# Kernel optimization log

Hardware: AMD Instinct MI355X
Metric: run time of the kernel (lower is better)

The kernel has to match this reference:

```python
import jax, jax.numpy as jnp
import numpy as np

TEMP = 0.1
EPS = 1e-8  # torch CosineSimilarity eps
B, C, T = 8, 256, 1024
M = 512    # masked positions per batch row (equal counts -> no padding branch)
K = 100    # negatives per masked position


def setup_inputs() -> dict:
    key = jax.random.key(0)
    k1, k2, k3 = jax.random.split(key, 3)
    context = jax.random.normal(k1, (B, C, T), dtype=jnp.float32)
    positive = jax.random.normal(k2, (B, C, T), dtype=jnp.float32)
    negatives = jax.random.normal(k3, (B, M, K, C), dtype=jnp.float32)
    # mask with exactly M True entries per row
    rng = np.random.default_rng(0)
    mask = np.zeros((B, T), dtype=bool)
    for b in range(B):
        mask[b, rng.permutation(T)[:M]] = True
    return {
        "context": context,
        "positive": positive,
        "negatives": negatives,
        "mask_indices": jnp.asarray(mask),
        "num_masked": M,
    }


def _cosine(a, b):
    # torch.nn.CosineSimilarity(dim=-1): dot / (max(|a|,eps) * max(|b|,eps))
    dot = jnp.sum(a * b, axis=-1)
    na = jnp.maximum(jnp.linalg.norm(a, axis=-1), EPS)
    nb = jnp.maximum(jnp.linalg.norm(b, axis=-1), EPS)
    return dot / (na * nb)


def reference(context, positive, negatives, mask_indices, num_masked):
    # [B,C,T] -> [B,T,C]
    ctx = jnp.transpose(context, (0, 2, 1))
    pos = jnp.transpose(positive, (0, 2, 1))
    # stable argsort puts masked positions first, preserving original order
    order = jnp.argsort(jnp.where(mask_indices, 0, 1), axis=1)  # [B,T]
    idx = order[:, :num_masked]                                 # [B,M]
    ctx_m = jnp.take_along_axis(ctx, idx[:, :, None], axis=1)   # [B,M,C]
    pos_m = jnp.take_along_axis(pos, idx[:, :, None], axis=1)   # [B,M,C]

    pos_sim = _cosine(ctx_m, pos_m)                    # [B,M]
    neg_sim = _cosine(ctx_m[:, :, None, :], negatives)  # [B,M,K]
    logits = jnp.concatenate([pos_sim[..., None], neg_sim], axis=-1) / TEMP  # [B,M,K+1]
    # cross-entropy with labels == 0, mean over B*M rows
    loss = jnp.mean(jax.nn.logsumexp(logits, axis=-1) - logits[..., 0])
    return loss
```

## Files before the change

### kernel.cpp

```cpp
#include <hip/hip_runtime.h>
#include <cstdint>

constexpr int Bb = 8;
constexpr int Cc = 256;
constexpr int Tt = 1024;
constexpr int Mm = 512;
constexpr int Kk = 100;
constexpr int PAIRS = 2;
constexpr int GRID  = (Bb * Mm) / PAIRS;
#define EPSF 1e-8f
#define INV_TEMP 10.0f

typedef float vf4 __attribute__((ext_vector_type(4)));

__global__ __launch_bounds__(1024)
void cl_mask_extract(const void* __restrict__ mask, int* __restrict__ idx) {
    const int b    = blockIdx.x;
    const int tid  = threadIdx.x;
    const int lane = tid & 63;
    const int wave = tid >> 6;

    __shared__ int wcnt8[16];
    __shared__ int wcnt32[16];
    __shared__ int wcntp[16];
    __shared__ int layout_s;

    const uint8_t* p8  = (const uint8_t*)mask;
    const int32_t* p32 = (const int32_t*)mask;
    unsigned long long bal8  = __ballot(p8[tid]  != 0);
    unsigned long long bal32 = __ballot(p32[tid] != 0);
    if (lane == 0) { wcnt8[wave] = __popcll(bal8); wcnt32[wave] = __popcll(bal32); }
    __syncthreads();
    if (tid == 0) {
        int c8 = 0, c32 = 0;
        for (int w = 0; w < 16; ++w) { c8 += wcnt8[w]; c32 += wcnt32[w]; }
        layout_s = (c8 == Mm) ? 1 : ((c32 == Mm) ? 4 : 8);
    }
    __syncthreads();
    const int esz = layout_s;

    const long long off = (long long)b * Tt + tid;
    int bit;
    if (esz == 1)      bit = (p8[off]  != 0);
    else if (esz == 4) bit = (p32[off] != 0);
    else               bit = (((const int64_t*)mask)[off] != 0);

    unsigned long long bp = __ballot(bit);
    if (lane == 0) wcntp[wave] = __popcll(bp);
    __syncthreads();
    int base = 0;
    for (int w = 0; w < wave; ++w) base += wcntp[w];
    const int rank = base + __popcll(bp & ((1ull << lane) - 1ull));
    if (bit && rank < Mm) idx[b * Mm + rank] = tid;
}

__global__ __launch_bounds__(256)
void cl_main(const float* __restrict__ context,
             const float* __restrict__ positive,
             const float* __restrict__ negatives,
             const int*   __restrict__ idx,
             float*       __restrict__ lossbuf) {
    const int g    = blockIdx.x;
    const int bm0  = g;
    const int bm1  = g + GRID;
    const int b0   = bm0 >> 9;
    const int b1   = bm1 >> 9;
    const int tid  = threadIdx.x;
    const int lane = tid & 63;
    const int wave = tid >> 6;
    const int q    = lane & 15;
    const int ks   = lane >> 4;

    __shared__ __align__(16) float ctx_s[2][Cc];
    __shared__ float redf[4][6];
    __shared__ float logits[2][Kk + 4];

    const int t0 = idx[bm0];
    const int t1 = idx[bm1];
    const float cv0 = context [((size_t)(b0 * Cc + tid)) * Tt + t0];
    const float pv0 = positive[((size_t)(b0 * Cc + tid)) * Tt + t0];
    const float cv1 = context [((size_t)(b1 * Cc + tid)) * Tt + t1];
    const float pv1 = positive[((size_t)(b1 * Cc + tid)) * Tt + t1];
    ctx_s[0][tid] = cv0;
    ctx_s[1][tid] = cv1;

    float s0 = cv0 * cv0, s1 = pv0 * pv0, s2 = cv0 * pv0;
    float s3 = cv1 * cv1, s4 = pv1 * pv1, s5 = cv1 * pv1;
    #pragma unroll
    for (int d = 32; d >= 1; d >>= 1) {
        s0 += __shfl_xor(s0, d); s1 += __shfl_xor(s1, d); s2 += __shfl_xor(s2, d);
        s3 += __shfl_xor(s3, d); s4 += __shfl_xor(s4, d); s5 += __shfl_xor(s5, d);
    }
    if (lane == 0) {
        redf[wave][0] = s0; redf[wave][1] = s1; redf[wave][2] = s2;
        redf[wave][3] = s3; redf[wave][4] = s4; redf[wave][5] = s5;
    }
    __syncthreads();

    const float4* c40 = (const float4*)ctx_s[0];
    const float4* c41 = (const float4*)ctx_s[1];
    float4 cr0[4], cr1[4];
    #pragma unroll
    for (int j = 0; j < 4; ++j) { cr0[j] = c40[j * 16 + q]; cr1[j] = c41[j * 16 + q]; }

    auto kloop = [&](const float4* cr, long long nbase, float* lrow) {
        #pragma unroll 2
        for (int it = 0; it < 7; ++it) {
            const int k = it * 16 + wave * 4 + ks;
            float dotp = 0.f, sq = 0.f;
            if (k < Kk) {
                const vf4* np4 = (const vf4*)(negatives + nbase + (long long)k * Cc);
                #pragma unroll
                for (int j = 0; j < 4; ++j) {
                    const vf4 nv = __builtin_nontemporal_load(np4 + j * 16 + q);
                    dotp += cr[j].x * nv.x + cr[j].y * nv.y + cr[j].z * nv.z + cr[j].w * nv.w;
                    sq   += nv.x * nv.x + nv.y * nv.y + nv.z * nv.z + nv.w * nv.w;
                }
            }
            #pragma unroll
            for (int d = 1; d <= 8; d <<= 1) {
                dotp += __shfl_xor(dotp, d);
                sq   += __shfl_xor(sq, d);
            }
            if (k < Kk && q == 0) {
                const float nb = fmaxf(sqrtf(sq), EPSF);
                lrow[1 + k] = dotp / nb;
            }
        }
    };

    auto lse = [&](const float* lrow, float na2, float np2, float dcp, int bm) {
        const float na = fmaxf(sqrtf(na2), EPSF);
        const float np = fmaxf(sqrtf(np2), EPSF);
        const float scale = INV_TEMP / na;
        const float a_raw = (lane == 0) ? (dcp / np) : lrow[lane];
        const float b_raw = (lane + 64 <= Kk) ? lrow[lane + 64] : -3e28f;
        const float a  = a_raw * scale;
        const float bb = b_raw * scale;
        float mx = fmaxf(a, bb);
        #pragma unroll
        for (int d = 32; d >= 1; d >>= 1) mx = fmaxf(mx, __shfl_xor(mx, d));
        float e = expf(a - mx) + expf(bb - mx);
        #pragma unroll
        for (int d = 32; d >= 1; d >>= 1) e += __shfl_xor(e, d);
        const float logit0 = __shfl(a, 0);
        if (lane == 0) lossbuf[bm] = mx + logf(e) - logit0;
    };

    kloop(cr0, (long long)bm0 * Kk * Cc, logits[0]);
    __syncthreads();

    if (wave == 0) {
        const float na2 = redf[0][0] + redf[1][0] + redf[2][0] + redf[3][0];
        const float np2 = redf[0][1] + redf[1][1] + redf[2][1] + redf[3][1];
        const float dcp = redf[0][2] + redf[1][2] + redf[2][2] + redf[3][2];
        lse(logits[0], na2, np2, dcp, bm0);
    }
    kloop(cr1, (long long)bm1 * Kk * Cc, logits[1]);
    __syncthreads();

    if (wave == 0) {
        const float na2 = redf[0][3] + redf[1][3] + redf[2][3] + redf[3][3];
        const float np2 = redf[0][4] + redf[1][4] + redf[2][4] + redf[3][4];
        const float dcp = redf[0][5] + redf[1][5] + redf[2][5] + redf[3][5];
        lse(logits[1], na2, np2, dcp, bm1);
    }
}

__global__ __launch_bounds__(256)
void cl_reduce(const float* __restrict__ lossbuf, float* __restrict__ out) {
    const int tid = threadIdx.x;
    float s = 0.f;
    #pragma unroll
    for (int i = 0; i < 16; ++i) s += lossbuf[tid * 16 + i];
    #pragma unroll
    for (int d = 32; d >= 1; d >>= 1) s += __shfl_xor(s, d);
    __shared__ float ws[4];
    if ((tid & 63) == 0) ws[tid >> 6] = s;
    __syncthreads();
    if (tid == 0) out[0] = (ws[0] + ws[1] + ws[2] + ws[3]) * (1.0f / (Bb * Mm));
}

extern "C" void kernel_launch(void* const* d_in, const int* in_sizes, int n_in,
                              void* d_out, int out_size, void* d_ws, size_t ws_size,
                              hipStream_t stream) {
    const float* context   = (const float*)d_in[0];
    const float* positive  = (const float*)d_in[1];
    const float* negatives = (const float*)d_in[2];
    const void*  mask      = d_in[3];

    int*   idx     = (int*)d_ws;
    float* lossbuf = (float*)(idx + Bb * Mm);

    cl_mask_extract<<<Bb, 1024, 0, stream>>>(mask, idx);
    cl_main<<<GRID, 256, 0, stream>>>(context, positive, negatives, idx, lossbuf);
    cl_reduce<<<1, 256, 0, stream>>>(lossbuf, (float*)d_out);
}
```

Measured before the change: 93.99 us.

## Fuse mask index extraction into main kernel and process adjacent positions per block

Removes the separate mask-extract kernel launch. Each main block now recomputes the layout detection and a prefix scan over its batch row's mask to find its two masked time indices. Blocks now handle two adjacent masked positions, so their negatives reads are contiguous. The final reduce is vectorized to float4 loads. The cost is redundant mask scanning in every block, plus two extra barriers before the gather.

```diff
diff --git a/kernel.cpp b/kernel.cpp
--- a/kernel.cpp
+++ b/kernel.cpp
@@ -6,65 +6,22 @@
 constexpr int Tt = 1024;
 constexpr int Mm = 512;
 constexpr int Kk = 100;
-constexpr int PAIRS = 2;
-constexpr int GRID  = (Bb * Mm) / PAIRS;
+constexpr int GRID = (Bb * Mm) / 2;
 #define EPSF 1e-8f
 #define INV_TEMP 10.0f
 
 typedef float vf4 __attribute__((ext_vector_type(4)));
-
-__global__ __launch_bounds__(1024)
-void cl_mask_extract(const void* __restrict__ mask, int* __restrict__ idx) {
-    const int b    = blockIdx.x;
-    const int tid  = threadIdx.x;
-    const int lane = tid & 63;
-    const int wave = tid >> 6;
-
-    __shared__ int wcnt8[16];
-    __shared__ int wcnt32[16];
-    __shared__ int wcntp[16];
-    __shared__ int layout_s;
-
-    const uint8_t* p8  = (const uint8_t*)mask;
-    const int32_t* p32 = (const int32_t*)mask;
-    unsigned long long bal8  = __ballot(p8[tid]  != 0);
-    unsigned long long bal32 = __ballot(p32[tid] != 0);
-    if (lane == 0) { wcnt8[wave] = __popcll(bal8); wcnt32[wave] = __popcll(bal32); }
-    __syncthreads();
-    if (tid == 0) {
-        int c8 = 0, c32 = 0;
-        for (int w = 0; w < 16; ++w) { c8 += wcnt8[w]; c32 += wcnt32[w]; }
-        layout_s = (c8 == Mm) ? 1 : ((c32 == Mm) ? 4 : 8);
-    }
-    __syncthreads();
-    const int esz = layout_s;
-
-    const long long off = (long long)b * Tt + tid;
-    int bit;
-    if (esz == 1)      bit = (p8[off]  != 0);
-    else if (esz == 4) bit = (p32[off] != 0);
-    else               bit = (((const int64_t*)mask)[off] != 0);
-
-    unsigned long long bp = __ballot(bit);
-    if (lane == 0) wcntp[wave] = __popcll(bp);
-    __syncthreads();
-    int base = 0;
-    for (int w = 0; w < wave; ++w) base += wcntp[w];
-    const int rank = base + __popcll(bp & ((1ull << lane) - 1ull));
-    if (bit && rank < Mm) idx[b * Mm + rank] = tid;
-}
 
 __global__ __launch_bounds__(256)
 void cl_main(const float* __restrict__ context,
              const float* __restrict__ positive,
              const float* __restrict__ negatives,
-             const int*   __restrict__ idx,
+             const void*  __restrict__ mask,
              float*       __restrict__ lossbuf) {
     const int g    = blockIdx.x;
-    const int bm0  = g;
-    const int bm1  = g + GRID;
-    const int b0   = bm0 >> 9;
-    const int b1   = bm1 >> 9;
+    const int bm0  = g * 2;
+    const int b    = bm0 >> 9;
+    const int m0   = bm0 & (Mm - 1);
     const int tid  = threadIdx.x;
     const int lane = tid & 63;
     const int wave = tid >> 6;
@@ -73,14 +30,76 @@
 
     __shared__ __align__(16) float ctx_s[2][Cc];
     __shared__ float redf[4][6];
+    __shared__ int   redi[4][2];
+    __shared__ int   scan_w[4];
     __shared__ float logits[2][Kk + 4];
-
-    const int t0 = idx[bm0];
-    const int t1 = idx[bm1];
-    const float cv0 = context [((size_t)(b0 * Cc + tid)) * Tt + t0];
-    const float pv0 = positive[((size_t)(b0 * Cc + tid)) * Tt + t0];
-    const float cv1 = context [((size_t)(b1 * Cc + tid)) * Tt + t1];
-    const float pv1 = positive[((size_t)(b1 * Cc + tid)) * Tt + t1];
+    __shared__ int   t_sh[2];
+
+    const uint8_t* p8  = (const uint8_t*)mask;
+    const int32_t* p32 = (const int32_t*)mask;
+
+    int c8 = 0, c32 = 0;
+    #pragma unroll
+    for (int j = 0; j < 4; ++j) {
+        c8  += (p8 [j * 256 + tid] != 0);
+        c32 += (p32[j * 256 + tid] != 0);
+    }
+    #pragma unroll
+    for (int d = 32; d >= 1; d >>= 1) { c8 += __shfl_xor(c8, d); c32 += __shfl_xor(c32, d); }
+    if (lane == 0) { redi[wave][0] = c8; redi[wave][1] = c32; }
+    __syncthreads();
+    const int tc8  = redi[0][0] + redi[1][0] + redi[2][0] + redi[3][0];
+    const int tc32 = redi[0][1] + redi[1][1] + redi[2][1] + redi[3][1];
+    const int esz  = (tc8 == Mm) ? 1 : ((tc32 == Mm) ? 4 : 8);
+
+    int bits = 0;
+    if (esz == 1) {
+        const uint32_t w = *(const uint32_t*)(p8 + (size_t)b * Tt + tid * 4);
+        bits = ((w & 0xffu)       ? 1 : 0) |
+               ((w & 0xff00u)     ? 2 : 0) |
+               ((w & 0xff0000u)   ? 4 : 0) |
+               ((w & 0xff000000u) ? 8 : 0);
+    } else if (esz == 4) {
+        #pragma unroll
+        for (int j = 0; j < 4; ++j)
+            bits |= (p32[(size_t)b * Tt + tid * 4 + j] != 0) << j;
+    } else {
+        const int64_t* p64 = (const int64_t*)mask;
+        #pragma unroll
+        for (int j = 0; j < 4; ++j)
+            bits |= (p64[(size_t)b * Tt + tid * 4 + j] != 0) << j;
+    }
+    const int cnt = __popc(bits);
+    int incl = cnt;
+    #pragma unroll
+    for (int d = 1; d < 64; d <<= 1) { const int v = __shfl_up(incl, d); if (lane >= d) incl += v; }
+    if (lane == 63) scan_w[wave] = incl;
+    __syncthreads();
+    int basec = 0;
+    for (int w = 0; w < wave; ++w) basec += scan_w[w];
+    incl += basec;
+    const int excl = incl - cnt;
+    #pragma unroll
+    for (int sel = 0; sel < 2; ++sel) {
+        const int mm = m0 + sel;
+        if (excl <= mm && mm < incl) {
+            int need = mm - excl;
+            #pragma unroll
+            for (int j = 0; j < 4; ++j) {
+                if ((bits >> j) & 1) { if (need == 0) t_sh[sel] = tid * 4 + j; --need; }
+            }
+        }
+    }
+    __syncthreads();
+    const int t0 = t_sh[0];
+    const int t1 = t_sh[1];
+
+    const float* crow = context  + (size_t)(b * Cc + tid) * Tt;
+    const float* prow = positive + (size_t)(b * Cc + tid) * Tt;
+    const float cv0 = crow[t0];
+    const float pv0 = prow[t0];
+    const float cv1 = crow[t1];
+    const float pv1 = prow[t1];
     ctx_s[0][tid] = cv0;
     ctx_s[1][tid] = cv1;
 
@@ -147,7 +166,9 @@
         if (lane == 0) lossbuf[bm] = mx + logf(e) - logit0;
     };
 
-    kloop(cr0, (long long)bm0 * Kk * Cc, logits[0]);
+    const long long nbase0 = (long long)bm0 * Kk * Cc;
+
+    kloop(cr0, nbase0, logits[0]);
     __syncthreads();
 
     if (wave == 0) {
@@ -156,14 +177,14 @@
         const float dcp = redf[0][2] + redf[1][2] + redf[2][2] + redf[3][2];
         lse(logits[0], na2, np2, dcp, bm0);
     }
-    kloop(cr1, (long long)bm1 * Kk * Cc, logits[1]);
+    kloop(cr1, nbase0 + (long long)Kk * Cc, logits[1]);
     __syncthreads();
 
     if (wave == 0) {
         const float na2 = redf[0][3] + redf[1][3] + redf[2][3] + redf[3][3];
         const float np2 = redf[0][4] + redf[1][4] + redf[2][4] + redf[3][4];
         const float dcp = redf[0][5] + redf[1][5] + redf[2][5] + redf[3][5];
-        lse(logits[1], na2, np2, dcp, bm1);
+        lse(logits[1], na2, np2, dcp, bm0 + 1);
     }
 }
 
@@ -172,7 +193,10 @@
     const int tid = threadIdx.x;
     float s = 0.f;
     #pragma unroll
-    for (int i = 0; i < 16; ++i) s += lossbuf[tid * 16 + i];
+    for (int i = 0; i < 4; ++i) {
+        const float4 v = *(const float4*)(lossbuf + tid * 16 + i * 4);
+        s += (v.x + v.y) + (v.z + v.w);
+    }
     #pragma unroll
     for (int d = 32; d >= 1; d >>= 1) s += __shfl_xor(s, d);
     __shared__ float ws[4];
@@ -189,10 +213,8 @@
     const float* negatives = (const float*)d_in[2];
     const void*  mask      = d_in[3];
 
-    int*   idx     = (int*)d_ws;
-    float* lossbuf = (float*)(idx + Bb * Mm);
-
-    cl_mask_extract<<<Bb, 1024, 0, stream>>>(mask, idx);
-    cl_main<<<GRID, 256, 0, stream>>>(context, positive, negatives, idx, lossbuf);
+    float* lossbuf = (float*)d_ws;
+
+    cl_main<<<GRID, 256, 0, stream>>>(context, positive, negatives, mask, lossbuf);
     cl_reduce<<<1, 256, 0, stream>>>(lossbuf, (float*)d_out);
 }
```

After: 90.69 us. 3.5% less time.
